# Performance work log

Hardware: AMD Instinct MI355X
Metric: run time of the kernel (lower is better)

Reference implementation:

```python
import jax, jax.numpy as jnp
import numpy as np

N_NODES = 100000


def setup_inputs() -> dict:
    key = jax.random.key(0)
    ks = jax.random.split(key, 9)
    E = 1600000
    x = jax.random.normal(ks[0], (N_NODES, 12), dtype=jnp.float32)
    edge_index = jax.random.randint(ks[1], (2, E), 0, N_NODES, dtype=jnp.int64)
    def glorot(k, shape):
        lim = float(np.sqrt(6.0 / (shape[0] + shape[1])))
        return jax.random.uniform(k, shape, jnp.float32, -lim, lim)
    return {
        "x": x,
        "edge_index": edge_index,
        "W1": glorot(ks[2], (12, 64)),
        "b1": jnp.zeros((64,), jnp.float32),
        "W2": glorot(ks[3], (64, 128)),
        "b2": jnp.zeros((128,), jnp.float32),
        "W3": glorot(ks[4], (128, 96)),
        "b3": jnp.zeros((96,), jnp.float32),
    }


def reference(x, edge_index, W1, b1, W2, b2, W3, b3):
    N = x.shape[0]
    F_channel, n_his = 8, 12
    src, dst = edge_index[0], edge_index[1]
    # add self loops (PyG GCNConv default)
    loop = jnp.arange(N, dtype=src.dtype)
    src = jnp.concatenate([src, loop])
    dst = jnp.concatenate([dst, loop])
    # symmetric normalization: norm_e = deg[src]^-1/2 * deg[dst]^-1/2
    deg = jax.ops.segment_sum(jnp.ones_like(src, dtype=x.dtype), dst, num_segments=N)
    dinv = jnp.where(deg > 0, jax.lax.rsqrt(deg), 0.0)
    norm = dinv[src] * dinv[dst]  # [E+N]

    def gcn(h, W, b):
        hw = h @ W  # transform first (out_ch <= in-edge fanout cost)
        agg = jax.ops.segment_sum(hw[src] * norm[:, None], dst, num_segments=N)
        return agg + b

    h = jax.nn.relu(gcn(x, W1, b1))
    h = jax.nn.relu(gcn(h, W2, b2))
    h = gcn(h, W3, b3)
    return h.reshape(N, F_channel, n_his)
```

## Files before the change

kernel.cpp:

```cpp
#include <hip/hip_runtime.h>
#include <hip/hip_bf16.h>
#include <hip/hip_fp16.h>


static inline int cdiv(int a, int b) { return (a + b - 1) / b; }
constexpr int BLOCK = 256;
constexpr int BSHIFT = 9;
constexpr int BNODES = 1 << BSHIFT;

typedef float nfloat4 __attribute__((ext_vector_type(4)));
typedef _Float16 f16x8 __attribute__((ext_vector_type(8)));
typedef float f32x16 __attribute__((ext_vector_type(16)));


__device__ __forceinline__ void nt_store_raw16(void* p, float4 v) {
    nfloat4 nv;
    nv.x = v.x; nv.y = v.y; nv.z = v.z; nv.w = v.w;
    __builtin_nontemporal_store(nv, (nfloat4*)p);
}

struct h4 { __half2 a, b; };
__device__ __forceinline__ void store_h4(__half* p, float4 v) {
    h4 r;
    r.a = __floats2half2_rn(v.x, v.y);
    r.b = __floats2half2_rn(v.z, v.w);
    *(h4*)p = r;
}

__device__ __forceinline__ void h8_add(float* acc, float4 raw) {
    union { float4 f; __half2 h[4]; } u;
    u.f = raw;
#pragma unroll
    for (int j = 0; j < 4; ++j) {
        float2 p = __half22float2(u.h[j]);
        acc[2 * j] += p.x;
        acc[2 * j + 1] += p.y;
    }
}


template <int CHUNK>
__global__ void bucket_count_kernel(const int* __restrict__ dst, int E,
                                    int* __restrict__ bcnt, int NB) {
    __shared__ int cnt[256];
    for (int i = threadIdx.x; i < NB; i += blockDim.x) cnt[i] = 0;
    __syncthreads();
    const int e0 = blockIdx.x * CHUNK;
    const int e1 = min(e0 + CHUNK, E);
    for (int e = e0 + threadIdx.x; e < e1; e += blockDim.x)
        atomicAdd(&cnt[dst[e] >> BSHIFT], 1);
    __syncthreads();
    for (int i = threadIdx.x; i < NB; i += blockDim.x)
        if (cnt[i]) atomicAdd(&bcnt[i], cnt[i]);
}

__global__ void bucket_scan_kernel(const int* __restrict__ bcnt, int* __restrict__ gbase,
                                   int* __restrict__ gcur, int NB) {
    __shared__ int tmp[256];
    int t = threadIdx.x;
    int v = (t < NB) ? bcnt[t] : 0;
    tmp[t] = v;
    __syncthreads();
    for (int off = 1; off < 256; off <<= 1) {
        int add = (t >= off) ? tmp[t - off] : 0;
        __syncthreads();
        tmp[t] += add;
        __syncthreads();
    }
    if (t < NB) { int ex = tmp[t] - v; gbase[t] = ex; gcur[t] = ex; }
}

template <int CHUNK>
__global__ void bin_edges_kernel(const int* __restrict__ ei, int E,
                                 int* __restrict__ gcur, unsigned* __restrict__ binned,
                                 int NB) {
    __shared__ int cnt[256], base[256], rk[256];
    for (int i = threadIdx.x; i < NB; i += blockDim.x) { cnt[i] = 0; rk[i] = 0; }
    __syncthreads();
    const int e0 = blockIdx.x * CHUNK;
    const int e1 = min(e0 + CHUNK, E);
    for (int e = e0 + threadIdx.x; e < e1; e += blockDim.x)
        atomicAdd(&cnt[ei[E + e] >> BSHIFT], 1);
    __syncthreads();
    for (int i = threadIdx.x; i < NB; i += blockDim.x)
        base[i] = atomicAdd(&gcur[i], cnt[i]);
    __syncthreads();
    for (int e = e0 + threadIdx.x; e < e1; e += blockDim.x) {
        int s = ei[e], d = ei[E + e];
        int b = d >> BSHIFT;
        int r = atomicAdd(&rk[b], 1);
        binned[base[b] + r] = (unsigned)s | ((unsigned)(d & (BNODES - 1)) << 17);
    }
}

__global__ void csr_fill_kernel(const int* __restrict__ gbase, const int* __restrict__ bcnt,
                                const unsigned* __restrict__ binned,
                                int* __restrict__ deg, float* __restrict__ dinv,
                                int* __restrict__ row_ptr, int* __restrict__ csr_src,
                                int* __restrict__ dh, int N) {
    __shared__ int c[BNODES];
    __shared__ int ps[256];
    __shared__ int dhloc[64];
    const int t = threadIdx.x;
    const int b = blockIdx.x;
    const int node0 = b << BSHIFT;
    if (t < BNODES) c[t] = 0;
    if (t < 64) dhloc[t] = 0;
    __syncthreads();
    const int base = gbase[b];
    const int end = base + bcnt[b];
    for (int e = base + t; e < end; e += 1024)
        atomicAdd(&c[binned[e] >> 17], 1);
    __syncthreads();
    int s0 = 0, s1 = 0;
    if (t < 256) {
        s0 = c[2 * t]; s1 = c[2 * t + 1];
        ps[t] = s0 + s1;
    }
    __syncthreads();
    for (int off = 1; off < 256; off <<= 1) {
        int add = (t >= off && t < 256) ? ps[t - off] : 0;
        __syncthreads();
        if (t < 256) ps[t] += add;
        __syncthreads();
    }
    if (t < 256) {
        const int ex = ps[t] - (s0 + s1);
        const int p0 = base + ex;
        const int p1 = p0 + s0;
        const int n0 = node0 + 2 * t;
        if (n0 < N) {
            row_ptr[n0] = p0; deg[n0] = s0; dinv[n0] = rsqrtf((float)s0 + 1.0f);
            atomicAdd(&dhloc[min(s0, 63)], 1);
            if (n0 + 1 < N) {
                row_ptr[n0 + 1] = p1; deg[n0 + 1] = s1; dinv[n0 + 1] = rsqrtf((float)s1 + 1.0f);
                atomicAdd(&dhloc[min(s1, 63)], 1);
            }
        }
        c[2 * t] = p0; c[2 * t + 1] = p1;
    }
    __syncthreads();
    if (t < 64 && dhloc[t]) atomicAdd(&dh[t], dhloc[t]);
    for (int e = base + t; e < end; e += 1024) {
        unsigned sd = binned[e];
        int pos = atomicAdd(&c[sd >> 17], 1);
        csr_src[pos] = (int)(sd & 0x1FFFFu);
    }
}


__global__ void dscan_kernel(int* __restrict__ dh) {
    __shared__ int tmp[64];
    int t = threadIdx.x;
    int v = dh[t];
    tmp[t] = v;
    __syncthreads();
    for (int off = 1; off < 64; off <<= 1) {
        int add = (t >= off) ? tmp[t - off] : 0;
        __syncthreads();
        tmp[t] += add;
        __syncthreads();
    }
    dh[t] = tmp[t] - v;
}

__global__ void dperm_kernel(const int* __restrict__ deg, const int* __restrict__ row_ptr,
                             const float* __restrict__ dinv, int* __restrict__ dh,
                             int4* __restrict__ hdr, int N) {
    __shared__ int cnt[64], base[64], rk[64];
    const int t = threadIdx.x;
    if (t < 64) { cnt[t] = 0; rk[t] = 0; }
    __syncthreads();
    const int i = blockIdx.x * blockDim.x + t;
    const int d = (i < N) ? deg[i] : 0;
    const int myb = (i < N) ? min(d, 63) : -1;
    if (myb >= 0) atomicAdd(&cnt[myb], 1);
    __syncthreads();
    if (t < 64) base[t] = cnt[t] ? atomicAdd(&dh[t], cnt[t]) : 0;
    __syncthreads();
    if (myb >= 0) {
        int r = atomicAdd(&rk[myb], 1);
        int slot = base[myb] + r;
        int4 h;
        h.x = row_ptr[i];
        h.y = d;
        h.z = i;
        h.w = __float_as_int(dinv[i]);
        hdr[N - 1 - slot] = h;
    }
}


__global__ void prescale_h_kernel(const float* __restrict__ x, const float* __restrict__ dinv,
                                  __half* __restrict__ xs, int N) {
    int i = blockIdx.x * blockDim.x + threadIdx.x;
    if (i >= N) return;
    float di = dinv[i];
    const float4* xr = (const float4*)(x + (size_t)i * 12);
    float4 a = xr[0], b = xr[1], c = xr[2];
    union { float4 f; __half2 h[4]; } u0, u1;
    u0.h[0] = __floats2half2_rn(a.x * di, a.y * di);
    u0.h[1] = __floats2half2_rn(a.z * di, a.w * di);
    u0.h[2] = __floats2half2_rn(b.x * di, b.y * di);
    u0.h[3] = __floats2half2_rn(b.z * di, b.w * di);
    u1.h[0] = __floats2half2_rn(c.x * di, c.y * di);
    u1.h[1] = __floats2half2_rn(c.z * di, c.w * di);
    u1.h[2] = __floats2half2_rn(0.f, 0.f);
    u1.h[3] = __floats2half2_rn(0.f, 0.f);
    float4* op = (float4*)(xs + (size_t)i * 16);
    op[0] = u0.f;
    op[1] = u1.f;
}


__global__ void gather_x_t1_kernel(const int4* __restrict__ hdr,
                                   const int* __restrict__ csr_src,
                                   const __half* __restrict__ xs,
                                   const float* __restrict__ W1,
                                   const float* __restrict__ b1,
                                   __half* __restrict__ h1h, int N) {
    __shared__ float W1s[12 * 64];
    __shared__ float xrow[128][12];
    const int tid = threadIdx.x;
    for (int u = tid; u < 12 * 64 / 4; u += 256)
        ((float4*)W1s)[u] = ((const float4*)W1)[u];

    const int t = blockIdx.x * 256 + tid;
    const bool valid = (t < N * 2);
    const int slot = t >> 1;
    const int c = t & 1;
    const int nl = tid >> 1;
    int4 H = valid ? hdr[slot] : make_int4(0, 0, 0, 0);
    const int* __restrict__ sp = csr_src + H.x;
    const int n = valid ? H.y : 0;
    const int i = H.z;
    const float di = __int_as_float(H.w);
    const int f0 = c * 8;

    float acc[8];
    {
        union { float4 f; __half2 h[4]; } u;
        u.f = *(const float4*)(xs + (size_t)i * 16 + f0);
#pragma unroll
        for (int j = 0; j < 4; ++j) {
            float2 p = __half22float2(u.h[j]);
            acc[2 * j] = p.x; acc[2 * j + 1] = p.y;
        }
    }

    int k = 0;
    if (n >= 8) {
        int s[8];
#pragma unroll
        for (int j = 0; j < 8; ++j) s[j] = sp[j];
        for (; k + 16 <= n; k += 8) {
            int ns[8];
#pragma unroll
            for (int j = 0; j < 8; ++j) ns[j] = sp[k + 8 + j];
            float4 v[8];
#pragma unroll
            for (int j = 0; j < 8; ++j) v[j] = *(const float4*)(xs + (size_t)s[j] * 16 + f0);
#pragma unroll
            for (int j = 0; j < 8; ++j) h8_add(acc, v[j]);
#pragma unroll
            for (int j = 0; j < 8; ++j) s[j] = ns[j];
        }
        float4 v[8];
#pragma unroll
        for (int j = 0; j < 8; ++j) v[j] = *(const float4*)(xs + (size_t)s[j] * 16 + f0);
#pragma unroll
        for (int j = 0; j < 8; ++j) h8_add(acc, v[j]);
        k += 8;
    }
    for (; k + 4 <= n; k += 4) {
        int s0 = sp[k + 0], s1 = sp[k + 1], s2 = sp[k + 2], s3 = sp[k + 3];
        float4 v0 = *(const float4*)(xs + (size_t)s0 * 16 + f0);
        float4 v1 = *(const float4*)(xs + (size_t)s1 * 16 + f0);
        float4 v2 = *(const float4*)(xs + (size_t)s2 * 16 + f0);
        float4 v3 = *(const float4*)(xs + (size_t)s3 * 16 + f0);
        h8_add(acc, v0); h8_add(acc, v1); h8_add(acc, v2); h8_add(acc, v3);
    }
    for (; k < n; ++k) {
        float4 v = *(const float4*)(xs + (size_t)sp[k] * 16 + f0);
        h8_add(acc, v);
    }

    if (valid) {
        if (c == 0) {
#pragma unroll
            for (int j = 0; j < 8; ++j) xrow[nl][j] = acc[j] * di;
        } else {
#pragma unroll
            for (int j = 0; j < 4; ++j) xrow[nl][8 + j] = acc[j] * di;
        }
    }
    __syncthreads();
    if (!valid) return;

    float xr[12];
#pragma unroll
    for (int j = 0; j < 12; ++j) xr[j] = xrow[nl][j];

    __half* op = h1h + (size_t)i * 64 + c * 32;
#pragma unroll
    for (int g = 0; g < 8; ++g) {
        const int c0 = c * 32 + g * 4;
        float4 r = *(const float4*)(b1 + c0);
#pragma unroll
        for (int kk = 0; kk < 12; ++kk) {
            const float4 w = *(const float4*)(W1s + kk * 64 + c0);
            r.x = fmaf(xr[kk], w.x, r.x);
            r.y = fmaf(xr[kk], w.y, r.y);
            r.z = fmaf(xr[kk], w.z, r.z);
            r.w = fmaf(xr[kk], w.w, r.w);
        }
        r.x = fmaxf(r.x, 0.f) * di; r.y = fmaxf(r.y, 0.f) * di;
        r.z = fmaxf(r.z, 0.f) * di; r.w = fmaxf(r.w, 0.f) * di;
        store_h4(op + g * 4, r);
    }
}


__global__ void prep_w_kernel(const float* __restrict__ W2, const float* __restrict__ W3,
                              __half* __restrict__ W2T, __half* __restrict__ W3T) {
    int i = blockIdx.x * 256 + threadIdx.x;
    if (i < 64 * 128) {
        int k = i >> 7, n = i & 127;
        W2T[n * 64 + k] = __float2half(W2[i]);
    } else {
        int j = i - 64 * 128;
        if (j < 128 * 96) {
            int k = j / 96, n = j - k * 96;
            W3T[n * 128 + k] = __float2half(W3[j]);
        }
    }
}

__global__ void __launch_bounds__(256, 3)
fused_g64_t2t3_kernel(const __half* __restrict__ h1h,
                      const int* __restrict__ row_ptr, const int* __restrict__ deg,
                      const int* __restrict__ csr_src, const float* __restrict__ dinv,
                      const __half* __restrict__ W2T,
                      const float* __restrict__ b2,
                      const __half* __restrict__ W3T,
                      __half* __restrict__ out,
                      int N) {
    constexpr int LDH = 136;
    __shared__ _Float16 h2s[4][32 * LDH];
    const int lane = threadIdx.x & 63;
    const int wid = threadIdx.x >> 6;
    const int l31 = lane & 31;
    const int lh = lane >> 5;
    _Float16* hs = h2s[wid];

    float b2v[4];
#pragma unroll
    for (int nt = 0; nt < 4; ++nt) b2v[nt] = b2[nt * 32 + l31];

    const int NT = N >> 5;
    for (int t = blockIdx.x * 4 + wid; t < NT; t += gridDim.x * 4) {
        const int r0 = t << 5;
        const int i = r0 + l31;

        float acc[32];
        {
            const char* rp = (const char*)h1h + (size_t)i * 128 + lh * 16;
#pragma unroll
            for (int kb = 0; kb < 4; ++kb) {
                union { float4 f; __half2 h[4]; } u;
                u.f = *(const float4*)(rp + kb * 32);
#pragma unroll
                for (int j = 0; j < 4; ++j) {
                    float2 p = __half22float2(u.h[j]);
                    acc[kb * 8 + 2 * j] = p.x;
                    acc[kb * 8 + 2 * j + 1] = p.y;
                }
            }
        }
        {
            const int* __restrict__ sp = csr_src + row_ptr[i];
            const int n = deg[i];
            if (n > 0) {
                int s = sp[0];
                int k = 0;
                for (; k + 1 < n; ++k) {
                    int s2 = sp[k + 1];
                    const char* p = (const char*)h1h + (size_t)s * 128 + lh * 16;
                    float4 v0 = *(const float4*)(p);
                    float4 v1 = *(const float4*)(p + 32);
                    float4 v2 = *(const float4*)(p + 64);
                    float4 v3 = *(const float4*)(p + 96);
                    h8_add(acc + 0, v0); h8_add(acc + 8, v1);
                    h8_add(acc + 16, v2); h8_add(acc + 24, v3);
                    s = s2;
                }
                const char* p = (const char*)h1h + (size_t)s * 128 + lh * 16;
                float4 v0 = *(const float4*)(p);
                float4 v1 = *(const float4*)(p + 32);
                float4 v2 = *(const float4*)(p + 64);
                float4 v3 = *(const float4*)(p + 96);
                h8_add(acc + 0, v0); h8_add(acc + 8, v1);
                h8_add(acc + 16, v2); h8_add(acc + 24, v3);
            }
        }
        f16x8 a2[4];
        {
            const float di = dinv[i];
#pragma unroll
            for (int kb = 0; kb < 4; ++kb)
#pragma unroll
                for (int j = 0; j < 8; ++j)
                    a2[kb][j] = (_Float16)(acc[kb * 8 + j] * di);
        }

#pragma unroll
        for (int nt = 0; nt < 4; ++nt) {
            f32x16 c = {0.f, 0.f, 0.f, 0.f, 0.f, 0.f, 0.f, 0.f,
                        0.f, 0.f, 0.f, 0.f, 0.f, 0.f, 0.f, 0.f};
#pragma unroll
            for (int kb = 0; kb < 4; ++kb) {
                f16x8 b = *(const f16x8*)(W2T + (size_t)(nt * 32 + l31) * 64 + kb * 16 + lh * 8);
                c = __builtin_amdgcn_mfma_f32_32x32x16_f16(a2[kb], b, c, 0, 0, 0);
            }
#pragma unroll
            for (int r = 0; r < 16; ++r) {
                int row = (r & 3) + 8 * (r >> 2) + 4 * lh;
                float v = fmaxf(c[r] + b2v[nt], 0.f);
                hs[row * LDH + nt * 32 + l31] = (_Float16)v;
            }
        }

        f16x8 a3[8];
#pragma unroll
        for (int kb = 0; kb < 8; ++kb)
            a3[kb] = *(const f16x8*)(hs + l31 * LDH + kb * 16 + lh * 8);
        float4 dv[4];
#pragma unroll
        for (int rg = 0; rg < 4; ++rg)
            dv[rg] = *(const float4*)(dinv + r0 + rg * 8 + lh * 4);
#pragma unroll
        for (int nt = 0; nt < 3; ++nt) {
            f32x16 c = {0.f, 0.f, 0.f, 0.f, 0.f, 0.f, 0.f, 0.f,
                        0.f, 0.f, 0.f, 0.f, 0.f, 0.f, 0.f, 0.f};
#pragma unroll
            for (int kb = 0; kb < 8; ++kb) {
                f16x8 b = *(const f16x8*)(W3T + (size_t)(nt * 32 + l31) * 128 + kb * 16 + lh * 8);
                c = __builtin_amdgcn_mfma_f32_32x32x16_f16(a3[kb], b, c, 0, 0, 0);
            }
#pragma unroll
            for (int r = 0; r < 16; ++r) {
                int row = (r & 3) + 8 * (r >> 2) + 4 * lh;
                float dvv = ((const float*)&dv[r >> 2])[r & 3];
                hs[row * LDH + nt * 32 + l31] = (_Float16)(c[r] * dvv);
            }
        }

#pragma unroll
        for (int it = 0; it < 6; ++it) {
            int id = lane + it * 64;
            int row = id / 12, ch = id - row * 12;
            float4 v = *(const float4*)(hs + row * LDH + ch * 8);
            *(float4*)((char*)(out + (size_t)r0 * 96) + (size_t)id * 16) = v;
        }
    }
}


template <int F, bool HAS_BIAS, bool OUT_HALF>
__global__ void gather_h_kernel(const int4* __restrict__ hdr, const int* __restrict__ csr_src,
                                const __half* __restrict__ hws,
                                const float* __restrict__ b, void* __restrict__ out_v, int N) {
    constexpr int TPN = F / 8;
    int t = blockIdx.x * blockDim.x + threadIdx.x;
    if (t >= N * TPN) return;
    int slot = t / TPN;
    int c = t - slot * TPN;
    const int4 H = hdr[slot];
    const int* __restrict__ sp = csr_src + H.x;
    const int n = H.y;
    const int i = H.z;
    const float di = __int_as_float(H.w);
    int f0 = c * 8;

    float acc[8];
    {
        union { float4 f; __half2 h[4]; } u;
        u.f = *(const float4*)(hws + (size_t)i * F + f0);
#pragma unroll
        for (int j = 0; j < 4; ++j) {
            float2 p = __half22float2(u.h[j]);
            acc[2 * j] = p.x; acc[2 * j + 1] = p.y;
        }
    }

    int k = 0;
    if (n >= 8) {
        int s[8];
#pragma unroll
        for (int j = 0; j < 8; ++j) s[j] = sp[j];
        for (; k + 16 <= n; k += 8) {
            int ns[8];
#pragma unroll
            for (int j = 0; j < 8; ++j) ns[j] = sp[k + 8 + j];
            float4 v[8];
#pragma unroll
            for (int j = 0; j < 8; ++j) v[j] = *(const float4*)(hws + (size_t)s[j] * F + f0);
#pragma unroll
            for (int j = 0; j < 8; ++j) h8_add(acc, v[j]);
#pragma unroll
            for (int j = 0; j < 8; ++j) s[j] = ns[j];
        }
        float4 v[8];
#pragma unroll
        for (int j = 0; j < 8; ++j) v[j] = *(const float4*)(hws + (size_t)s[j] * F + f0);
#pragma unroll
        for (int j = 0; j < 8; ++j) h8_add(acc, v[j]);
        k += 8;
    }
    for (; k + 4 <= n; k += 4) {
        int s0 = sp[k + 0], s1 = sp[k + 1], s2 = sp[k + 2], s3 = sp[k + 3];
        float4 v0 = *(const float4*)(hws + (size_t)s0 * F + f0);
        float4 v1 = *(const float4*)(hws + (size_t)s1 * F + f0);
        float4 v2 = *(const float4*)(hws + (size_t)s2 * F + f0);
        float4 v3 = *(const float4*)(hws + (size_t)s3 * F + f0);
        h8_add(acc, v0); h8_add(acc, v1); h8_add(acc, v2); h8_add(acc, v3);
    }
    for (; k < n; ++k) {
        float4 v = *(const float4*)(hws + (size_t)sp[k] * F + f0);
        h8_add(acc, v);
    }

    float4 r0, r1;
    if (HAS_BIAS) {
        const float4 bb0 = *(const float4*)(b + f0);
        const float4 bb1 = *(const float4*)(b + f0 + 4);
        r0.x = fmaf(acc[0], di, bb0.x); r0.y = fmaf(acc[1], di, bb0.y);
        r0.z = fmaf(acc[2], di, bb0.z); r0.w = fmaf(acc[3], di, bb0.w);
        r1.x = fmaf(acc[4], di, bb1.x); r1.y = fmaf(acc[5], di, bb1.y);
        r1.z = fmaf(acc[6], di, bb1.z); r1.w = fmaf(acc[7], di, bb1.w);
    } else {
        r0.x = acc[0] * di; r0.y = acc[1] * di; r0.z = acc[2] * di; r0.w = acc[3] * di;
        r1.x = acc[4] * di; r1.y = acc[5] * di; r1.z = acc[6] * di; r1.w = acc[7] * di;
    }
    if (OUT_HALF) {
        union { float4 f; __half2 h[4]; } u;
        u.h[0] = __floats2half2_rn(r0.x, r0.y);
        u.h[1] = __floats2half2_rn(r0.z, r0.w);
        u.h[2] = __floats2half2_rn(r1.x, r1.y);
        u.h[3] = __floats2half2_rn(r1.z, r1.w);
        nt_store_raw16((__half*)out_v + (size_t)i * F + f0, u.f);
    } else {
        float* op = (float*)out_v + (size_t)i * F + f0;
        nt_store_raw16(op, r0);
        nt_store_raw16(op + 4, r1);
    }
}


extern "C" void kernel_launch(void* const* d_in, const int* in_sizes, int n_in,
                              void* d_out, int out_size, void* d_ws, size_t ws_size,
                              hipStream_t stream) {
    const float* x  = (const float*)d_in[0];
    const int*   ei = (const int*)d_in[1];
    const float* W1 = (const float*)d_in[2];
    const float* b1 = (const float*)d_in[3];
    const float* W2 = (const float*)d_in[4];
    const float* b2 = (const float*)d_in[5];
    const float* W3 = (const float*)d_in[6];
    const float* b3 = (const float*)d_in[7];
    float* out = (float*)d_out;

    const int N = in_sizes[0] / 12;
    const int E = in_sizes[1] / 2;
    const int NB = cdiv(N, BNODES);

    char* ws = (char*)d_ws;
    int*   deg     = (int*)ws;    ws += (size_t)N * sizeof(int);
    int*   row_ptr = (int*)ws;    ws += (size_t)N * sizeof(int);
    int*   bcnt    = (int*)ws;    ws += 256 * sizeof(int);
    int*   dh      = (int*)ws;    ws += 64 * sizeof(int);
    int*   gbase   = (int*)ws;    ws += 256 * sizeof(int);
    int*   gcur    = (int*)ws;    ws += 256 * sizeof(int);
    float* dinv    = (float*)ws;  ws += (size_t)N * sizeof(float);
    int4*  hdr     = (int4*)ws;   ws += (size_t)N * sizeof(int4);
    __half* W2Th   = (__half*)ws; ws += 128 * 64 * sizeof(__half);
    __half* W3Th   = (__half*)ws; ws += 96 * 128 * sizeof(__half);
    int*   csr_src = (int*)ws;    ws += (size_t)E * sizeof(int);
    float* bufA    = (float*)ws;  ws += (size_t)N * 128 * sizeof(float);
    float* bufB    = (float*)ws;
    unsigned* binned = (unsigned*)bufB;

    hipMemsetAsync(bcnt, 0, (256 + 64) * sizeof(int), stream);
    prep_w_kernel<<<80, 256, 0, stream>>>(W2, W3, W2Th, W3Th);
    bucket_count_kernel<8192><<<cdiv(E, 8192), BLOCK, 0, stream>>>(ei + E, E, bcnt, NB);
    bucket_scan_kernel<<<1, 256, 0, stream>>>(bcnt, gbase, gcur, NB);
    bin_edges_kernel<8192><<<cdiv(E, 8192), BLOCK, 0, stream>>>(ei, E, gcur, binned, NB);
    csr_fill_kernel<<<NB, 1024, 0, stream>>>(gbase, bcnt, binned, deg, dinv, row_ptr,
                                             csr_src, dh, N);

    dscan_kernel<<<1, 64, 0, stream>>>(dh);
    dperm_kernel<<<cdiv(N, BLOCK), BLOCK, 0, stream>>>(deg, row_ptr, dinv, dh, hdr, N);

    prescale_h_kernel<<<cdiv(N, BLOCK), BLOCK, 0, stream>>>(x, dinv, (__half*)bufA, N);
    gather_x_t1_kernel<<<cdiv(N * 2, BLOCK), BLOCK, 0, stream>>>(
        hdr, csr_src, (const __half*)bufA, W1, b1, (__half*)bufB, N);

    fused_g64_t2t3_kernel<<<cdiv(N / 32, 4), 256, 0, stream>>>(
        (const __half*)bufB, row_ptr, deg, csr_src, dinv, W2Th, b2, W3Th,
        (__half*)bufA, N);

    gather_h_kernel<96, true, false><<<cdiv(N * 12, BLOCK), BLOCK, 0, stream>>>(
        hdr, csr_src, (const __half*)bufA, b3, out, N);
}
```

Measured before the change: 326.4 us.

## Split fused layer-2 gather across 8 threads per node with batched neighbor loads

The fused gather+GEMM kernel previously had 2 lanes per node, each loading 64 bytes per neighbor. Now a block-wide phase gives each node 8 threads with one 16-byte chunk each, prefetches 8 neighbor indices at a time, and stages the aggregated rows in shared memory before a barrier and the per-wave MFMA stages. The grid-stride loop is gone, so each block handles exactly 4 tiles, and launch bounds drop to 2 blocks per SM. This should raise memory-level parallelism and spread skewed node degrees across more threads. It depends on the host launching enough blocks to cover every tile, and it adds a block barrier and per-block launch overhead.

```diff
diff --git a/kernel.cpp b/kernel.cpp
--- a/kernel.cpp
+++ b/kernel.cpp
@@ -336,7 +336,7 @@
     }
 }
 
-__global__ void __launch_bounds__(256, 3)
+__global__ void __launch_bounds__(256, 2)
 fused_g64_t2t3_kernel(const __half* __restrict__ h1h,
                       const int* __restrict__ row_ptr, const int* __restrict__ deg,
                       const int* __restrict__ csr_src, const float* __restrict__ dinv,
@@ -346,122 +346,147 @@
                       __half* __restrict__ out,
                       int N) {
     constexpr int LDH = 136;
-    __shared__ _Float16 h2s[4][32 * LDH];
-    const int lane = threadIdx.x & 63;
-    const int wid = threadIdx.x >> 6;
+    __shared__ _Float16 buf[4][32 * LDH];
+    const int tid = threadIdx.x;
+    const int lane = tid & 63;
+    const int wid = tid >> 6;
     const int l31 = lane & 31;
     const int lh = lane >> 5;
-    _Float16* hs = h2s[wid];
-
-    float b2v[4];
-#pragma unroll
-    for (int nt = 0; nt < 4; ++nt) b2v[nt] = b2[nt * 32 + l31];
-
     const int NT = N >> 5;
-    for (int t = blockIdx.x * 4 + wid; t < NT; t += gridDim.x * 4) {
-        const int r0 = t << 5;
-        const int i = r0 + l31;
-
-        float acc[32];
-        {
-            const char* rp = (const char*)h1h + (size_t)i * 128 + lh * 16;
-#pragma unroll
-            for (int kb = 0; kb < 4; ++kb) {
+    const int t0 = blockIdx.x * 4;
+
+    {
+        const int nr = tid >> 3;
+        const int f0 = (tid & 7) * 8;
+#pragma unroll 1
+        for (int p = 0; p < 4; ++p) {
+            const int t = t0 + p;
+            if (t >= NT) break;
+            const int i = (t << 5) + nr;
+            const int* __restrict__ sp = csr_src + row_ptr[i];
+            const int n = deg[i];
+            const float di = dinv[i];
+
+            float acc[8];
+            {
                 union { float4 f; __half2 h[4]; } u;
-                u.f = *(const float4*)(rp + kb * 32);
+                u.f = *(const float4*)(h1h + (size_t)i * 64 + f0);
 #pragma unroll
                 for (int j = 0; j < 4; ++j) {
-                    float2 p = __half22float2(u.h[j]);
-                    acc[kb * 8 + 2 * j] = p.x;
-                    acc[kb * 8 + 2 * j + 1] = p.y;
+                    float2 pp = __half22float2(u.h[j]);
+                    acc[2 * j] = pp.x; acc[2 * j + 1] = pp.y;
                 }
             }
-        }
-        {
-            const int* __restrict__ sp = csr_src + row_ptr[i];
-            const int n = deg[i];
-            if (n > 0) {
-                int s = sp[0];
-                int k = 0;
-                for (; k + 1 < n; ++k) {
-                    int s2 = sp[k + 1];
-                    const char* p = (const char*)h1h + (size_t)s * 128 + lh * 16;
-                    float4 v0 = *(const float4*)(p);
-                    float4 v1 = *(const float4*)(p + 32);
-                    float4 v2 = *(const float4*)(p + 64);
-                    float4 v3 = *(const float4*)(p + 96);
-                    h8_add(acc + 0, v0); h8_add(acc + 8, v1);
-                    h8_add(acc + 16, v2); h8_add(acc + 24, v3);
-                    s = s2;
+
+            int k = 0;
+            if (n >= 8) {
+                int s[8];
+#pragma unroll
+                for (int j = 0; j < 8; ++j) s[j] = sp[j];
+                for (; k + 16 <= n; k += 8) {
+                    int ns[8];
+#pragma unroll
+                    for (int j = 0; j < 8; ++j) ns[j] = sp[k + 8 + j];
+                    float4 v[8];
+#pragma unroll
+                    for (int j = 0; j < 8; ++j) v[j] = *(const float4*)(h1h + (size_t)s[j] * 64 + f0);
+#pragma unroll
+                    for (int j = 0; j < 8; ++j) h8_add(acc, v[j]);
+#pragma unroll
+                    for (int j = 0; j < 8; ++j) s[j] = ns[j];
                 }
-                const char* p = (const char*)h1h + (size_t)s * 128 + lh * 16;
-                float4 v0 = *(const float4*)(p);
-                float4 v1 = *(const float4*)(p + 32);
-                float4 v2 = *(const float4*)(p + 64);
-                float4 v3 = *(const float4*)(p + 96);
-                h8_add(acc + 0, v0); h8_add(acc + 8, v1);
-                h8_add(acc + 16, v2); h8_add(acc + 24, v3);
+                float4 v[8];
+#pragma unroll
+                for (int j = 0; j < 8; ++j) v[j] = *(const float4*)(h1h + (size_t)s[j] * 64 + f0);
+#pragma unroll
+                for (int j = 0; j < 8; ++j) h8_add(acc, v[j]);
+                k += 8;
             }
-        }
-        f16x8 a2[4];
-        {
-            const float di = dinv[i];
-#pragma unroll
-            for (int kb = 0; kb < 4; ++kb)
-#pragma unroll
-                for (int j = 0; j < 8; ++j)
-                    a2[kb][j] = (_Float16)(acc[kb * 8 + j] * di);
-        }
-
-#pragma unroll
-        for (int nt = 0; nt < 4; ++nt) {
-            f32x16 c = {0.f, 0.f, 0.f, 0.f, 0.f, 0.f, 0.f, 0.f,
-                        0.f, 0.f, 0.f, 0.f, 0.f, 0.f, 0.f, 0.f};
-#pragma unroll
-            for (int kb = 0; kb < 4; ++kb) {
-                f16x8 b = *(const f16x8*)(W2T + (size_t)(nt * 32 + l31) * 64 + kb * 16 + lh * 8);
-                c = __builtin_amdgcn_mfma_f32_32x32x16_f16(a2[kb], b, c, 0, 0, 0);
+            for (; k + 4 <= n; k += 4) {
+                int s0 = sp[k + 0], s1 = sp[k + 1], s2 = sp[k + 2], s3 = sp[k + 3];
+                float4 v0 = *(const float4*)(h1h + (size_t)s0 * 64 + f0);
+                float4 v1 = *(const float4*)(h1h + (size_t)s1 * 64 + f0);
+                float4 v2 = *(const float4*)(h1h + (size_t)s2 * 64 + f0);
+                float4 v3 = *(const float4*)(h1h + (size_t)s3 * 64 + f0);
+                h8_add(acc, v0); h8_add(acc, v1); h8_add(acc, v2); h8_add(acc, v3);
             }
-#pragma unroll
-            for (int r = 0; r < 16; ++r) {
-                int row = (r & 3) + 8 * (r >> 2) + 4 * lh;
-                float v = fmaxf(c[r] + b2v[nt], 0.f);
-                hs[row * LDH + nt * 32 + l31] = (_Float16)v;
+            for (; k < n; ++k) {
+                float4 v = *(const float4*)(h1h + (size_t)sp[k] * 64 + f0);
+                h8_add(acc, v);
             }
-        }
-
-        f16x8 a3[8];
-#pragma unroll
-        for (int kb = 0; kb < 8; ++kb)
-            a3[kb] = *(const f16x8*)(hs + l31 * LDH + kb * 16 + lh * 8);
-        float4 dv[4];
-#pragma unroll
-        for (int rg = 0; rg < 4; ++rg)
-            dv[rg] = *(const float4*)(dinv + r0 + rg * 8 + lh * 4);
-#pragma unroll
-        for (int nt = 0; nt < 3; ++nt) {
-            f32x16 c = {0.f, 0.f, 0.f, 0.f, 0.f, 0.f, 0.f, 0.f,
-                        0.f, 0.f, 0.f, 0.f, 0.f, 0.f, 0.f, 0.f};
-#pragma unroll
-            for (int kb = 0; kb < 8; ++kb) {
-                f16x8 b = *(const f16x8*)(W3T + (size_t)(nt * 32 + l31) * 128 + kb * 16 + lh * 8);
-                c = __builtin_amdgcn_mfma_f32_32x32x16_f16(a3[kb], b, c, 0, 0, 0);
-            }
-#pragma unroll
-            for (int r = 0; r < 16; ++r) {
-                int row = (r & 3) + 8 * (r >> 2) + 4 * lh;
-                float dvv = ((const float*)&dv[r >> 2])[r & 3];
-                hs[row * LDH + nt * 32 + l31] = (_Float16)(c[r] * dvv);
-            }
-        }
-
-#pragma unroll
-        for (int it = 0; it < 6; ++it) {
-            int id = lane + it * 64;
-            int row = id / 12, ch = id - row * 12;
-            float4 v = *(const float4*)(hs + row * LDH + ch * 8);
-            *(float4*)((char*)(out + (size_t)r0 * 96) + (size_t)id * 16) = v;
-        }
+
+            union { float4 f; __half2 h[4]; } o;
+            o.h[0] = __floats2half2_rn(acc[0] * di, acc[1] * di);
+            o.h[1] = __floats2half2_rn(acc[2] * di, acc[3] * di);
+            o.h[2] = __floats2half2_rn(acc[4] * di, acc[5] * di);
+            o.h[3] = __floats2half2_rn(acc[6] * di, acc[7] * di);
+            *(float4*)(&buf[p][nr * LDH + f0]) = o.f;
+        }
+    }
+    __syncthreads();
+
+    const int t = t0 + wid;
+    if (t >= NT) return;
+    const int r0 = t << 5;
+    _Float16* hs = buf[wid];
+
+    float b2v[4];
+#pragma unroll
+    for (int nt = 0; nt < 4; ++nt) b2v[nt] = b2[nt * 32 + l31];
+
+    f16x8 a2[4];
+#pragma unroll
+    for (int kb = 0; kb < 4; ++kb)
+        a2[kb] = *(const f16x8*)(hs + l31 * LDH + kb * 16 + lh * 8);
+
+#pragma unroll
+    for (int nt = 0; nt < 4; ++nt) {
+        f32x16 c = {0.f, 0.f, 0.f, 0.f, 0.f, 0.f, 0.f, 0.f,
+                    0.f, 0.f, 0.f, 0.f, 0.f, 0.f, 0.f, 0.f};
+#pragma unroll
+        for (int kb = 0; kb < 4; ++kb) {
+            f16x8 b = *(const f16x8*)(W2T + (size_t)(nt * 32 + l31) * 64 + kb * 16 + lh * 8);
+            c = __builtin_amdgcn_mfma_f32_32x32x16_f16(a2[kb], b, c, 0, 0, 0);
+        }
+#pragma unroll
+        for (int r = 0; r < 16; ++r) {
+            int row = (r & 3) + 8 * (r >> 2) + 4 * lh;
+            float v = fmaxf(c[r] + b2v[nt], 0.f);
+            hs[row * LDH + nt * 32 + l31] = (_Float16)v;
+        }
+    }
+
+    f16x8 a3[8];
+#pragma unroll
+    for (int kb = 0; kb < 8; ++kb)
+        a3[kb] = *(const f16x8*)(hs + l31 * LDH + kb * 16 + lh * 8);
+    float4 dv[4];
+#pragma unroll
+    for (int rg = 0; rg < 4; ++rg)
+        dv[rg] = *(const float4*)(dinv + r0 + rg * 8 + lh * 4);
+#pragma unroll
+    for (int nt = 0; nt < 3; ++nt) {
+        f32x16 c = {0.f, 0.f, 0.f, 0.f, 0.f, 0.f, 0.f, 0.f,
+                    0.f, 0.f, 0.f, 0.f, 0.f, 0.f, 0.f, 0.f};
+#pragma unroll
+        for (int kb = 0; kb < 8; ++kb) {
+            f16x8 b = *(const f16x8*)(W3T + (size_t)(nt * 32 + l31) * 128 + kb * 16 + lh * 8);
+            c = __builtin_amdgcn_mfma_f32_32x32x16_f16(a3[kb], b, c, 0, 0, 0);
+        }
+#pragma unroll
+        for (int r = 0; r < 16; ++r) {
+            int row = (r & 3) + 8 * (r >> 2) + 4 * lh;
+            float dvv = ((const float*)&dv[r >> 2])[r & 3];
+            hs[row * LDH + nt * 32 + l31] = (_Float16)(c[r] * dvv);
+        }
+    }
+
+#pragma unroll
+    for (int it = 0; it < 6; ++it) {
+        int id = lane + it * 64;
+        int row = id / 12, ch = id - row * 12;
+        float4 v = *(const float4*)(hs + row * LDH + ch * 8);
+        *(float4*)((char*)(out + (size_t)r0 * 96) + (size_t)id * 16) = v;
     }
 }
 
```

After: 276.2 us. 1.18x faster.
